# Performance work log

Hardware: AMD Instinct MI355X
Metric: run time of the kernel (lower is better)

## Reference

```python
import jax, jax.numpy as jnp
import numpy as np


def _chamfer_single_directional(x, y):
    """Mean over batch of mean over points of min_j ||x_i - y_j||^2.

    x: [B, N, 3] (predicted), y: [B, M, 3] (target).
    Matches pytorch3d chamfer_distance(x, y, single_directional=True)
    with norm=2, point_reduction='mean', batch_reduction='mean'.
    """
    x2 = jnp.sum(x * x, axis=-1)                      # [B, N]
    y2 = jnp.sum(y * y, axis=-1)                      # [B, M]
    cross = jnp.einsum('bnd,bmd->bnm', x, y)          # [B, N, M]
    d2 = x2[:, :, None] + y2[:, None, :] - 2.0 * cross  # squared L2
    min_d2 = jnp.min(d2, axis=2)                      # [B, N] nearest in y
    return jnp.mean(jnp.mean(min_d2, axis=1))         # scalar


def setup_inputs() -> dict:
    key = jax.random.key(0)
    k1, k2 = jax.random.split(key)
    v = jax.random.normal(k1, (4, 8192, 3), dtype=jnp.float32)
    v_pred = jax.random.normal(k2, (4, 8192, 3), dtype=jnp.float32)
    return {"v": v, "v_pred": v_pred}


def reference(v, v_pred):
    # forward: chamfer_distance(v_pred, v, single_directional=True)
    return _chamfer_single_directional(v_pred, v)
```

## Files before the change

### kernel.cpp

```cpp
#include <hip/hip_runtime.h>

#define BB 4
#define NN 8192
#define MM 8192
#define BN (BB * NN)

#define BLK 256
#define P   8
#define NX  (BLK*P)
#define S   64
#define MC  (MM/S)

#define KEY_C 128.0f

__global__ __launch_bounds__(BLK) void chamfer_min_atomic(
    const float* __restrict__ y,
    const float* __restrict__ x,
    int* __restrict__ gkey)
{
    __shared__ float4 zb[MC];
    const int t  = threadIdx.x;
    const int ib = blockIdx.x;
    const int s  = blockIdx.y;
    const int b  = blockIdx.z;

    const float* yb = y + ((size_t)b * MM + (size_t)s * MC) * 3;
    if (t < MC) {
        float y0 = yb[3*t + 0];
        float y1 = yb[3*t + 1];
        float y2 = yb[3*t + 2];
        zb[t] = make_float4(2.0f*y0, 2.0f*y1, 2.0f*y2,
                            __builtin_fmaf(y2, y2, __builtin_fmaf(y1, y1, y0*y0)));
    }
    __syncthreads();

    float x0[P], x1[P], x2[P], xx[P], best[P];
    const float* xb = x + ((size_t)b * NN + (size_t)ib * NX) * 3;
#pragma unroll
    for (int p = 0; p < P; ++p) {
        int i = t + p * BLK;
        x0[p] = xb[3*i + 0];
        x1[p] = xb[3*i + 1];
        x2[p] = xb[3*i + 2];
        xx[p] = __builtin_fmaf(x2[p], x2[p], __builtin_fmaf(x1[p], x1[p], x0[p]*x0[p]));
        best[p] = 3.4e38f;
    }

#pragma unroll 4
    for (int j = 0; j < MC; ++j) {
        float4 z = zb[j];
#pragma unroll
        for (int p = 0; p < P; ++p) {
            float tt = __builtin_fmaf(-x0[p], z.x, z.w);
            tt = __builtin_fmaf(-x1[p], z.y, tt);
            tt = __builtin_fmaf(-x2[p], z.z, tt);
            best[p] = fminf(best[p], tt);
        }
    }

    int* gk = gkey + (size_t)b * NN + (size_t)ib * NX;
#pragma unroll
    for (int p = 0; p < P; ++p) {
        float d2  = best[p] + xx[p];
        float key = KEY_C - d2;
        atomicMax(&gk[t + p * BLK], __float_as_int(key));
    }
}

__global__ __launch_bounds__(1024) void final_sum(
    const int* __restrict__ gkey,
    float* __restrict__ out)
{
    const int t = threadIdx.x;
    float acc = 0.0f;
#pragma unroll 4
    for (int i = t; i < BN; i += 1024) {
        acc += KEY_C - __int_as_float(gkey[i]);
    }
    for (int off = 32; off > 0; off >>= 1) {
        acc += __shfl_down(acc, off, 64);
    }
    __shared__ float wsum[16];
    const int lane = t & 63;
    const int w    = t >> 6;
    if (lane == 0) wsum[w] = acc;
    __syncthreads();
    if (t == 0) {
        float tot = 0.0f;
#pragma unroll
        for (int i = 0; i < 16; ++i) tot += wsum[i];
        out[0] = tot * (1.0f / (float)BN);
    }
}

extern "C" void kernel_launch(void* const* d_in, const int* in_sizes, int n_in,
                              void* d_out, int out_size, void* d_ws, size_t ws_size,
                              hipStream_t stream) {
    const float* v      = (const float*)d_in[0];
    const float* v_pred = (const float*)d_in[1];
    float* out = (float*)d_out;

    int* gkey = (int*)d_ws;

    dim3 grid1(NN / NX, S, BB);
    chamfer_min_atomic<<<grid1, BLK, 0, stream>>>(v, v_pred, gkey);

    final_sum<<<1, 1024, 0, stream>>>(gkey, out);
}
```

Baseline: 78.58 us.

## Use packed FP32 FMA with SoA shared layout and larger per-thread tile

```diff
diff --git a/kernel.cpp b/kernel.cpp
--- a/kernel.cpp
+++ b/kernel.cpp
@@ -6,19 +6,34 @@
 #define BN (BB * NN)
 
 #define BLK 256
-#define P   8
+#define P   16
 #define NX  (BLK*P)
 #define S   64
 #define MC  (MM/S)
 
 #define KEY_C 128.0f
 
+typedef float v2f __attribute__((ext_vector_type(2)));
+
+#if defined(__has_builtin) && __has_builtin(__builtin_elementwise_fma)
+#define VFMA(a, b, c) __builtin_elementwise_fma((a), (b), (c))
+#else
+static __device__ inline v2f VFMA(v2f a, v2f b, v2f c) {
+    v2f r; r.x = __builtin_fmaf(a.x, b.x, c.x); r.y = __builtin_fmaf(a.y, b.y, c.y);
+    return r;
+}
+#endif
+
 __global__ __launch_bounds__(BLK) void chamfer_min_atomic(
     const float* __restrict__ y,
     const float* __restrict__ x,
     int* __restrict__ gkey)
 {
-    __shared__ float4 zb[MC];
+    __shared__ __attribute__((aligned(16))) float ZX[MC];
+    __shared__ __attribute__((aligned(16))) float ZY[MC];
+    __shared__ __attribute__((aligned(16))) float ZZ[MC];
+    __shared__ __attribute__((aligned(16))) float ZW[MC];
+
     const int t  = threadIdx.x;
     const int ib = blockIdx.x;
     const int s  = blockIdx.y;
@@ -29,32 +44,48 @@
         float y0 = yb[3*t + 0];
         float y1 = yb[3*t + 1];
         float y2 = yb[3*t + 2];
-        zb[t] = make_float4(2.0f*y0, 2.0f*y1, 2.0f*y2,
-                            __builtin_fmaf(y2, y2, __builtin_fmaf(y1, y1, y0*y0)));
+        ZX[t] = 2.0f * y0;
+        ZY[t] = 2.0f * y1;
+        ZZ[t] = 2.0f * y2;
+        ZW[t] = __builtin_fmaf(y2, y2, __builtin_fmaf(y1, y1, y0*y0));
     }
     __syncthreads();
 
-    float x0[P], x1[P], x2[P], xx[P], best[P];
+    float nx0[P], nx1[P], nx2[P], xx[P], best[P];
     const float* xb = x + ((size_t)b * NN + (size_t)ib * NX) * 3;
 #pragma unroll
     for (int p = 0; p < P; ++p) {
         int i = t + p * BLK;
-        x0[p] = xb[3*i + 0];
-        x1[p] = xb[3*i + 1];
-        x2[p] = xb[3*i + 2];
-        xx[p] = __builtin_fmaf(x2[p], x2[p], __builtin_fmaf(x1[p], x1[p], x0[p]*x0[p]));
+        float a0 = xb[3*i + 0];
+        float a1 = xb[3*i + 1];
+        float a2 = xb[3*i + 2];
+        nx0[p] = -a0; nx1[p] = -a1; nx2[p] = -a2;
+        xx[p] = __builtin_fmaf(a2, a2, __builtin_fmaf(a1, a1, a0*a0));
         best[p] = 3.4e38f;
     }
 
-#pragma unroll 4
-    for (int j = 0; j < MC; ++j) {
-        float4 z = zb[j];
+    for (int jj = 0; jj < MC; jj += 4) {
+        float4 ax = ((const float4*)ZX)[jj >> 2];
+        float4 ay = ((const float4*)ZY)[jj >> 2];
+        float4 az = ((const float4*)ZZ)[jj >> 2];
+        float4 aw = ((const float4*)ZW)[jj >> 2];
+        v2f zx01 = {ax.x, ax.y}, zx23 = {ax.z, ax.w};
+        v2f zy01 = {ay.x, ay.y}, zy23 = {ay.z, ay.w};
+        v2f zz01 = {az.x, az.y}, zz23 = {az.z, az.w};
+        v2f zw01 = {aw.x, aw.y}, zw23 = {aw.z, aw.w};
 #pragma unroll
         for (int p = 0; p < P; ++p) {
-            float tt = __builtin_fmaf(-x0[p], z.x, z.w);
-            tt = __builtin_fmaf(-x1[p], z.y, tt);
-            tt = __builtin_fmaf(-x2[p], z.z, tt);
-            best[p] = fminf(best[p], tt);
+            v2f s0 = {nx0[p], nx0[p]};
+            v2f s1 = {nx1[p], nx1[p]};
+            v2f s2 = {nx2[p], nx2[p]};
+            v2f t01 = VFMA(s0, zx01, zw01);
+            t01 = VFMA(s1, zy01, t01);
+            t01 = VFMA(s2, zz01, t01);
+            v2f t23 = VFMA(s0, zx23, zw23);
+            t23 = VFMA(s1, zy23, t23);
+            t23 = VFMA(s2, zz23, t23);
+            float m = fminf(fminf(t01.x, t01.y), fminf(t23.x, t23.y));
+            best[p] = fminf(best[p], m);
         }
     }
 
@@ -72,10 +103,13 @@
     float* __restrict__ out)
 {
     const int t = threadIdx.x;
+    const int4* g4 = (const int4*)gkey;
     float acc = 0.0f;
-#pragma unroll 4
-    for (int i = t; i < BN; i += 1024) {
-        acc += KEY_C - __int_as_float(gkey[i]);
+#pragma unroll
+    for (int i = t; i < BN / 4; i += 1024) {
+        int4 k = g4[i];
+        acc += (KEY_C - __int_as_float(k.x)) + (KEY_C - __int_as_float(k.y))
+             + (KEY_C - __int_as_float(k.z)) + (KEY_C - __int_as_float(k.w));
     }
     for (int off = 32; off > 0; off >>= 1) {
         acc += __shfl_down(acc, off, 64);
```

After: 80.65 us. +2.6%, slower.
